# Kernel optimization log

Measured on AMD Instinct MI355X. Metric: run time of the kernel, lower is better.

Reference implementation:

```python
import jax, jax.numpy as jnp
import numpy as np

N = 32768      # nodes
E = 262144     # edges (avg degree 8)
D = 128        # d_model (= per-head out_channels, concat=False)
H = 4          # heads
C = D          # out_channels per head
R = 64         # rel_dim (edge_dim)
NREL = 64      # n_rels
L = 2          # num_layers
LEAK = 0.2     # GATv2 leaky_relu slope
LN_EPS = 1e-5


def setup_inputs() -> dict:
    key = jax.random.key(0)
    ks = jax.random.split(key, 12)
    sdD = 1.0 / np.sqrt(D)
    sdR = 1.0 / np.sqrt(R)
    return {
        "x_flat": jax.random.normal(ks[0], (N, D), jnp.float32),
        "edge_index": jax.random.randint(ks[1], (2, E), 0, N, jnp.int64),
        "edge_type": jax.random.randint(ks[2], (E,), 0, NREL, jnp.int64),
        "valid_mask_flat": jnp.ones((N,), bool),
        "rel_emb": jax.random.normal(ks[3], (NREL, R), jnp.float32) * 0.1,
        "Wl": jax.random.normal(ks[4], (L, D, H * C), jnp.float32) * sdD,
        "bl": jnp.zeros((L, H * C), jnp.float32),
        "Wr": jax.random.normal(ks[5], (L, D, H * C), jnp.float32) * sdD,
        "br": jnp.zeros((L, H * C), jnp.float32),
        "We": jax.random.normal(ks[6], (L, R, H * C), jnp.float32) * sdR,
        "att": jax.random.normal(ks[7], (L, H, C), jnp.float32) * 0.1,
        "bias_o": jnp.zeros((L, D), jnp.float32),
        "ln_g": jnp.ones((L, D), jnp.float32),
        "ln_b": jnp.zeros((L, D), jnp.float32),
    }


def _gatv2_layer(h, src, dst, ea, Wl, bl, Wr, br, We, att, b):
    # h: [N,D]; src/dst: [E+N]; ea: [E+N,R] edge embeddings (incl. self loops)
    xl = (h @ Wl + bl).reshape(N, H, C)   # source transform
    xr = (h @ Wr + br).reshape(N, H, C)   # target transform
    ep = (ea @ We).reshape(-1, H, C)
    e = jax.nn.leaky_relu(xl[src] + xr[dst] + ep, LEAK)   # [E+N,H,C]
    logits = jnp.einsum('ehc,hc->eh', e, att)             # [E+N,H]
    # segment softmax over destination node
    m = jax.ops.segment_max(logits, dst, num_segments=N)
    m = jnp.where(jnp.isfinite(m), m, 0.0)
    p = jnp.exp(logits - m[dst])
    denom = jax.ops.segment_sum(p, dst, num_segments=N)
    alpha = p / (denom[dst] + 1e-16)                      # [E+N,H]
    out = jax.ops.segment_sum(alpha[:, :, None] * xl[src], dst, num_segments=N)
    return out.mean(axis=1) + b                           # concat=False -> head mean


def reference(x_flat, edge_index, edge_type, valid_mask_flat,
              rel_emb, Wl, bl, Wr, br, We, att, bias_o, ln_g, ln_b):
    x = jnp.where(valid_mask_flat[:, None], x_flat, 0.0)
    src, dst = edge_index[0], edge_index[1]
    ea = rel_emb[edge_type]                               # [E,R]
    # PyG add_self_loops with fill_value='mean': self-loop edge_attr is the
    # mean of incoming edge attrs per target node (0 if no incoming edges).
    ones = jnp.ones((E,), x.dtype)
    deg = jax.ops.segment_sum(ones, dst, num_segments=N)
    self_attr = jax.ops.segment_sum(ea, dst, num_segments=N) / jnp.maximum(deg, 1.0)[:, None]
    loop = jnp.arange(N, dtype=src.dtype)
    src_f = jnp.concatenate([src, loop])
    dst_f = jnp.concatenate([dst, loop])
    ea_f = jnp.concatenate([ea, self_attr], axis=0)

    h = x
    for l in range(L):
        msg = _gatv2_layer(h, src_f, dst_f, ea_f,
                           Wl[l], bl[l], Wr[l], br[l], We[l], att[l], bias_o[l])
        msg = jax.nn.gelu(msg, approximate=False)         # dropout = identity (eval)
        hn = h + msg
        mu = jnp.mean(hn, axis=-1, keepdims=True)
        var = jnp.mean(jnp.square(hn - mu), axis=-1, keepdims=True)
        h = (hn - mu) / jnp.sqrt(var + LN_EPS) * ln_g[l] + ln_b[l]
    return jnp.where(valid_mask_flat[:, None], h, 0.0)
```

## Files before the change

### kernel.cpp

```cpp
#include <hip/hip_runtime.h>
#include <hip/hip_bf16.h>
#include <math.h>

#define NN 32768
#define EE 262144
#define DM 128
#define HH 4
#define CC 128
#define HC 512
#define RD 64
#define NRELS 64
#define LEAKS 0.2f
#define LNEPS 1e-5f
#define PIPE_L 4

typedef __hip_bfloat16 bf16;
typedef __attribute__((ext_vector_type(8))) short short8;
typedef __attribute__((ext_vector_type(4))) float f32x4;

typedef const __attribute__((address_space(1))) void* as1cv;
typedef __attribute__((address_space(3))) void* as3v;

__device__ __forceinline__ void gload16(const void* g, void* l) {
    __builtin_amdgcn_global_load_lds((as1cv)g, (as3v)l, 16, 0, 0);
}

__device__ __forceinline__ void unpack8(uint4 u, float* f) {
    f[0] = __uint_as_float((u.x & 0xffffu) << 16);
    f[1] = __uint_as_float(u.x & 0xffff0000u);
    f[2] = __uint_as_float((u.y & 0xffffu) << 16);
    f[3] = __uint_as_float(u.y & 0xffff0000u);
    f[4] = __uint_as_float((u.z & 0xffffu) << 16);
    f[5] = __uint_as_float(u.z & 0xffff0000u);
    f[6] = __uint_as_float((u.w & 0xffffu) << 16);
    f[7] = __uint_as_float(u.w & 0xffff0000u);
}

__global__ void k_deg(const int* __restrict__ dst, int* __restrict__ deg) {
    int e = blockIdx.x * 1024 + threadIdx.x;
    atomicAdd(&deg[dst[e]], 1);
}

__global__ void k_scan1(const int* __restrict__ deg, int* __restrict__ rowptr,
                        int* __restrict__ bsum) {
    __shared__ int s[256];
    int b = blockIdx.x, t = threadIdx.x;
    int v = deg[b * 256 + t];
    s[t] = v;
    __syncthreads();
    for (int off = 1; off < 256; off <<= 1) {
        int x = (t >= off) ? s[t - off] : 0;
        __syncthreads();
        s[t] += x;
        __syncthreads();
    }
    rowptr[b * 256 + t] = s[t] - v;
    if (t == 255) bsum[b] = s[255];
}

__global__ void k_small(const int* __restrict__ bsum, int* __restrict__ boff,
                        const int* __restrict__ hist, int* __restrict__ bcur) {
    __shared__ int s[128];
    int t = threadIdx.x;
    if (blockIdx.x == 0) {
        if (t < 128) s[t] = bsum[t];
        __syncthreads();
        for (int off = 1; off < 128; off <<= 1) {
            int x = (t >= off && t < 128) ? s[t - off] : 0;
            __syncthreads();
            if (t < 128) s[t] += x;
            __syncthreads();
        }
        if (t < 128) boff[t] = s[t] - bsum[t];
        if (t == 127) boff[128] = s[127];
    } else {
        if (t < 64) s[t] = hist[t];
        __syncthreads();
        for (int off = 1; off < 64; off <<= 1) {
            int x = (t >= off && t < 64) ? s[t - off] : 0;
            __syncthreads();
            if (t < 64) s[t] += x;
            __syncthreads();
        }
        if (t < 64) bcur[t] = s[t] - hist[t];
    }
}

__global__ void k_s3p(int* __restrict__ rowptr, const int* __restrict__ boff,
                      const int* __restrict__ deg, int* __restrict__ bcur,
                      int* __restrict__ perm) {
    __shared__ int lh[64], lbase[64];
    int t = threadIdx.x;
    int i = blockIdx.x * 256 + t;
    rowptr[i] += boff[i >> 8];
    if (i == NN - 1) rowptr[NN] = boff[128];
    if (t < 64) lh[t] = 0;
    __syncthreads();
    int d = deg[i];
    int b = 63 - (d > 63 ? 63 : d);
    int my = atomicAdd(&lh[b], 1);
    __syncthreads();
    if (t < 64 && lh[t] > 0) lbase[t] = atomicAdd(&bcur[t], lh[t]);
    __syncthreads();
    perm[lbase[b] + my] = i;
}

__global__ void k_hist(const int* __restrict__ deg, int* __restrict__ hist) {
    __shared__ int lh[64];
    int t = threadIdx.x;
    if (t < 64) lh[t] = 0;
    __syncthreads();
    int d = deg[blockIdx.x * 256 + t];
    int b = 63 - (d > 63 ? 63 : d);
    atomicAdd(&lh[b], 1);
    __syncthreads();
    if (t < 64 && lh[t] > 0) atomicAdd(&hist[t], lh[t]);
}

__global__ void k_fill(const int* __restrict__ src, const int* __restrict__ dst,
                       const int* __restrict__ etype, const int* __restrict__ rowptr,
                       int* __restrict__ cursor, unsigned* __restrict__ csr) {
    int e = blockIdx.x * 1024 + threadIdx.x;
    int d = dst[e];
    int pos = atomicAdd(&cursor[d], 1);
    csr[rowptr[d] + pos] = (unsigned)src[e] | ((unsigned)etype[e] << 16);
}

__global__ void k_prep(const float* __restrict__ x, bf16* __restrict__ hb,
                       const float* __restrict__ Wl, const float* __restrict__ Wr,
                       bf16* __restrict__ Wt,
                       const float* __restrict__ rel_emb, const float* __restrict__ We,
                       bf16* __restrict__ wep) {
    __shared__ float sa[RD];
    int b = blockIdx.x, tid = threadIdx.x;
    if (b < 2048) {
        int i = b * 256 + tid;
        const float4* p = (const float4*)x;
        float4 f0 = p[i * 2], f1 = p[i * 2 + 1];
        bf16 o[8];
        o[0] = __float2bfloat16(f0.x); o[1] = __float2bfloat16(f0.y);
        o[2] = __float2bfloat16(f0.z); o[3] = __float2bfloat16(f0.w);
        o[4] = __float2bfloat16(f1.x); o[5] = __float2bfloat16(f1.y);
        o[6] = __float2bfloat16(f1.z); o[7] = __float2bfloat16(f1.w);
        *reinterpret_cast<uint4*>(hb + (size_t)i * 8) = *reinterpret_cast<uint4*>(o);
    } else if (b < 3072) {
        int idx = (b - 2048) * 256 + tid;
        int l = idx >> 17;
        int rem = idx & 131071;
        int k = rem >> 10;
        int c = rem & 1023;
        const float* WlL = Wl + (size_t)l * DM * HC;
        const float* WrL = Wr + (size_t)l * DM * HC;
        float v = (c < HC) ? WlL[k * HC + c] : WrL[k * HC + (c - HC)];
        Wt[(size_t)l * 1024 * DM + (size_t)c * DM + k] = __float2bfloat16(v);
    } else {
        int blk = b - 3072;
        int l = blk >> 6, r = blk & 63;
        const float* WeL = We + (size_t)l * RD * HC;
        if (tid < RD) sa[tid] = rel_emb[r * RD + tid];
        __syncthreads();
        for (int c = tid; c < HC; c += 256) {
            float s = 0.f;
#pragma unroll 8
            for (int k = 0; k < RD; ++k) s += sa[k] * WeL[k * HC + c];
            wep[(size_t)l * NRELS * HC + (size_t)r * HC + c] = __float2bfloat16(s);
        }
    }
}

__global__ __launch_bounds__(256) void k_gemm_mfma(
    const bf16* __restrict__ hb, const bf16* __restrict__ Wt,
    const float* __restrict__ bl, const float* __restrict__ br,
    bf16* __restrict__ xlb, bf16* __restrict__ xrb) {
    int lane = threadIdx.x & 63;
    int wave = threadIdx.x >> 6;
    int rbase = blockIdx.x * 32;
    int lr = lane & 15;
    int lk = lane >> 4;
    const short* ha = (const short*)hb;
    const short* wa = (const short*)Wt;

    short8 a[2][4];
#pragma unroll
    for (int mi = 0; mi < 2; ++mi)
#pragma unroll
        for (int kk = 0; kk < 4; ++kk)
            a[mi][kk] = *(const short8*)(ha + (size_t)(rbase + mi * 16 + lr) * DM + kk * 32 + lk * 8);

    for (int cg = 0; cg < 4; ++cg) {
        int cbase = cg * 256 + wave * 64;
        short8 b[4][4];
#pragma unroll
        for (int ni = 0; ni < 4; ++ni)
#pragma unroll
            for (int kk = 0; kk < 4; ++kk)
                b[ni][kk] = *(const short8*)(wa + (size_t)(cbase + ni * 16 + lr) * DM + kk * 32 + lk * 8);

        f32x4 c[2][4];
#pragma unroll
        for (int mi = 0; mi < 2; ++mi)
#pragma unroll
            for (int ni = 0; ni < 4; ++ni)
                c[mi][ni] = (f32x4){0.f, 0.f, 0.f, 0.f};

#pragma unroll
        for (int kk = 0; kk < 4; ++kk)
#pragma unroll
            for (int mi = 0; mi < 2; ++mi)
#pragma unroll
                for (int ni = 0; ni < 4; ++ni)
                    c[mi][ni] = __builtin_amdgcn_mfma_f32_16x16x32_bf16(
                        a[mi][kk], b[ni][kk], c[mi][ni], 0, 0, 0);

#pragma unroll
        for (int ni = 0; ni < 4; ++ni) {
            int col = cbase + ni * 16 + lr;
            float bv = (col < HC) ? bl[col] : br[col - HC];
            bf16* outp;
            int cc;
            if (col < HC) { outp = xlb; cc = col; } else { outp = xrb; cc = col - HC; }
#pragma unroll
            for (int mi = 0; mi < 2; ++mi) {
#pragma unroll
                for (int r = 0; r < 4; ++r) {
                    int row = rbase + mi * 16 + lk * 4 + r;
                    outp[(size_t)row * HC + cc] = __float2bfloat16(c[mi][ni][r] + bv);
                }
            }
        }
    }
}

__global__ void k_node(
    const bf16* __restrict__ xlb, const bf16* __restrict__ xrb,
    const bf16* __restrict__ wep,
    const unsigned* __restrict__ csr, const int* __restrict__ rowptr,
    const int* __restrict__ perm,
    const float* __restrict__ attL, const float* __restrict__ biasL,
    const float* __restrict__ lngL, const float* __restrict__ lnbL,
    const float* __restrict__ h_in, float* __restrict__ h_out,
    bf16* __restrict__ hb_out) {
    __shared__ uint4 smem[4 * 528];
    int tid = threadIdx.x;
    int lane = tid & 63;
    int wave = tid >> 6;
    uint4* wls = smem + wave * 528;
    unsigned* csrS = (unsigned*)wls;
    unsigned char* ring = (unsigned char*)(wls + 16);

    int n = perm[blockIdx.x * 4 + wave];
    int head = lane >> 4;
    const int g0 = lane * 8;
    const int ch0 = (lane & 15) * 8;
    const short* xla = (const short*)xlb;
    const short* wpa = (const short*)wep;

    int r0 = rowptr[n], r1 = rowptr[n + 1];
    int d = r1 - r0;
    int de = (d < 64) ? d : 64;

    if (lane < de) csrS[lane] = csr[r0 + lane];

    float attv[8];
    {
        const float4* ap = (const float4*)(attL + head * CC + ch0);
        float4 a0 = ap[0], a1 = ap[1];
        attv[0] = a0.x; attv[1] = a0.y; attv[2] = a0.z; attv[3] = a0.w;
        attv[4] = a1.x; attv[5] = a1.y; attv[6] = a1.z; attv[7] = a1.w;
    }
    float xrn[8];
    unpack8(*(const uint4*)((const short*)xrb + (size_t)n * HC + g0), xrn);

    asm volatile("s_waitcnt vmcnt(0) lgkmcnt(0)" ::: "memory");
    __builtin_amdgcn_sched_barrier(0);

    float denom = 0.f;
    float acc[8], wpsum[8];
#pragma unroll
    for (int j = 0; j < 8; ++j) { acc[j] = 0.f; wpsum[j] = 0.f; }

    int npre = (de < PIPE_L) ? de : PIPE_L;
    for (int k = 0; k < npre; ++k) {
        unsigned u = csrS[k];
        unsigned char* slot = ring + (k & (PIPE_L - 1)) * 2048;
        gload16(xla + (size_t)(u & 0xffffu) * HC + lane * 8, slot);
        gload16(wpa + (size_t)(u >> 16) * HC + lane * 8, slot + 1024);
    }

    int i = 0;
    for (; i + PIPE_L < de; ++i) {
        asm volatile("s_waitcnt vmcnt(6)" ::: "memory");
        __builtin_amdgcn_sched_barrier(0);
        unsigned char* slot = ring + (i & (PIPE_L - 1)) * 2048;
        uint4 xv = *(const uint4*)(slot + lane * 16);
        uint4 wv = *(const uint4*)(slot + 1024 + lane * 16);
        asm volatile("s_waitcnt lgkmcnt(0)" ::: "memory");
        __builtin_amdgcn_sched_barrier(0);
        {
            unsigned u = csrS[i + PIPE_L];
            gload16(xla + (size_t)(u & 0xffffu) * HC + lane * 8, slot);
            gload16(wpa + (size_t)(u >> 16) * HC + lane * 8, slot + 1024);
        }
        float xs[8], wp[8];
        unpack8(xv, xs);
        unpack8(wv, wp);
        float p2 = 0.f;
#pragma unroll
        for (int j = 0; j < 8; ++j) {
            wpsum[j] += wp[j];
            float v = xs[j] + xrn[j] + wp[j];
            v = fmaxf(v, LEAKS * v);
            p2 += v * attv[j];
        }
        p2 += __shfl_xor(p2, 1);
        p2 += __shfl_xor(p2, 2);
        p2 += __shfl_xor(p2, 4);
        p2 += __shfl_xor(p2, 8);
        float pe = __expf(fminf(p2, 80.f));
        denom += pe;
#pragma unroll
        for (int j = 0; j < 8; ++j) acc[j] += pe * xs[j];
    }
    asm volatile("s_waitcnt vmcnt(0)" ::: "memory");
    __builtin_amdgcn_sched_barrier(0);
    for (; i < de; ++i) {
        unsigned char* slot = ring + (i & (PIPE_L - 1)) * 2048;
        uint4 xv = *(const uint4*)(slot + lane * 16);
        uint4 wv = *(const uint4*)(slot + 1024 + lane * 16);
        float xs[8], wp[8];
        unpack8(xv, xs);
        unpack8(wv, wp);
        float p2 = 0.f;
#pragma unroll
        for (int j = 0; j < 8; ++j) {
            wpsum[j] += wp[j];
            float v = xs[j] + xrn[j] + wp[j];
            v = fmaxf(v, LEAKS * v);
            p2 += v * attv[j];
        }
        p2 += __shfl_xor(p2, 1);
        p2 += __shfl_xor(p2, 2);
        p2 += __shfl_xor(p2, 4);
        p2 += __shfl_xor(p2, 8);
        float pe = __expf(fminf(p2, 80.f));
        denom += pe;
#pragma unroll
        for (int j = 0; j < 8; ++j) acc[j] += pe * xs[j];
    }

    for (int k = 64; k < d; ++k) {
        unsigned u = csr[r0 + k];
        uint4 xv = *(const uint4*)(xla + (size_t)(u & 0xffffu) * HC + g0);
        uint4 wv = *(const uint4*)(wpa + (size_t)(u >> 16) * HC + g0);
        float xs[8], wp[8];
        unpack8(xv, xs);
        unpack8(wv, wp);
        float p2 = 0.f;
#pragma unroll
        for (int j = 0; j < 8; ++j) {
            wpsum[j] += wp[j];
            float v = xs[j] + xrn[j] + wp[j];
            v = fmaxf(v, LEAKS * v);
            p2 += v * attv[j];
        }
        p2 += __shfl_xor(p2, 1);
        p2 += __shfl_xor(p2, 2);
        p2 += __shfl_xor(p2, 4);
        p2 += __shfl_xor(p2, 8);
        float pe = __expf(fminf(p2, 80.f));
        denom += pe;
#pragma unroll
        for (int j = 0; j < 8; ++j) acc[j] += pe * xs[j];
    }

    float xln[8];
    unpack8(*(const uint4*)(xla + (size_t)n * HC + g0), xln);
    float invd = (d > 0) ? (1.0f / (float)d) : 1.0f;
    float p2 = 0.f;
#pragma unroll
    for (int j = 0; j < 8; ++j) {
        float v = xln[j] + xrn[j] + wpsum[j] * invd;
        v = fmaxf(v, LEAKS * v);
        p2 += v * attv[j];
    }
    p2 += __shfl_xor(p2, 1);
    p2 += __shfl_xor(p2, 2);
    p2 += __shfl_xor(p2, 4);
    p2 += __shfl_xor(p2, 8);
    {
        float pe = __expf(fminf(p2, 80.f));
        denom += pe;
#pragma unroll
        for (int j = 0; j < 8; ++j) acc[j] += pe * xln[j];
    }

    float inv = 1.0f / (denom + 1e-16f);
    const float4* hp = (const float4*)(h_in + (size_t)n * DM + ch0);
    float4 h0 = hp[0], h1 = hp[1];
    float hin[8] = {h0.x, h0.y, h0.z, h0.w, h1.x, h1.y, h1.z, h1.w};
    float hn[8];
    float lsum = 0.f, lsq = 0.f;
#pragma unroll
    for (int j = 0; j < 8; ++j) {
        float v = acc[j] * inv;
        v += __shfl_xor(v, 16);
        v += __shfl_xor(v, 32);
        float x = v * 0.25f + biasL[ch0 + j];
        float ge = 0.5f * x * (1.0f + erff(x * 0.70710678f));
        float hv = hin[j] + ge;
        hn[j] = hv;
        lsum += hv;
        lsq += hv * hv;
    }
    lsum += __shfl_xor(lsum, 1);
    lsum += __shfl_xor(lsum, 2);
    lsum += __shfl_xor(lsum, 4);
    lsum += __shfl_xor(lsum, 8);
    lsq += __shfl_xor(lsq, 1);
    lsq += __shfl_xor(lsq, 2);
    lsq += __shfl_xor(lsq, 4);
    lsq += __shfl_xor(lsq, 8);
    float mu = lsum * (1.0f / 128.f);
    float var = lsq * (1.0f / 128.f) - mu * mu;
    float rstd = rsqrtf(var + LNEPS);
    if (lane < 16) {
#pragma unroll
        for (int j = 0; j < 8; ++j) {
            float o = (hn[j] - mu) * rstd * lngL[ch0 + j] + lnbL[ch0 + j];
            h_out[(size_t)n * DM + ch0 + j] = o;
            if (hb_out) hb_out[(size_t)n * DM + ch0 + j] = __float2bfloat16(o);
        }
    }
}

extern "C" void kernel_launch(void* const* d_in, const int* in_sizes, int n_in,
                              void* d_out, int out_size, void* d_ws, size_t ws_size,
                              hipStream_t stream) {
    const float* x_flat   = (const float*)d_in[0];
    const int*   edge_idx = (const int*)d_in[1];
    const int*   edge_typ = (const int*)d_in[2];
    const float* rel_emb  = (const float*)d_in[4];
    const float* Wl       = (const float*)d_in[5];
    const float* bl       = (const float*)d_in[6];
    const float* Wr       = (const float*)d_in[7];
    const float* br       = (const float*)d_in[8];
    const float* We       = (const float*)d_in[9];
    const float* att      = (const float*)d_in[10];
    const float* bias_o   = (const float*)d_in[11];
    const float* ln_g     = (const float*)d_in[12];
    const float* ln_b     = (const float*)d_in[13];

    const int* srcp = edge_idx;
    const int* dstp = edge_idx + EE;

    char* w = (char*)d_ws;
    auto alloc = [&](size_t bytes) -> void* {
        void* p = (void*)w;
        w += (bytes + 255) & ~(size_t)255;
        return p;
    };
    bf16*  xlb    = (bf16*)alloc((size_t)NN * HC * 2);
    bf16*  xrb    = (bf16*)alloc((size_t)NN * HC * 2);
    bf16*  hb     = (bf16*)alloc((size_t)NN * DM * 2);
    float* h_mid  = (float*)alloc((size_t)NN * DM * 4);
    bf16*  wep    = (bf16*)alloc((size_t)2 * NRELS * HC * 2);
    bf16*  Wt     = (bf16*)alloc((size_t)2 * 1024 * DM * 2);
    int*   deg    = (int*)alloc((size_t)NN * 4);
    int*   cursor = (int*)alloc((size_t)NN * 4);
    int*   hist   = (int*)alloc((size_t)64 * 4);
    int*   bcur   = (int*)alloc((size_t)64 * 4);
    int*   rowptr = (int*)alloc((size_t)(NN + 1) * 4);
    int*   bsum   = (int*)alloc((size_t)128 * 4);
    int*   boff   = (int*)alloc((size_t)129 * 4);
    int*   perm   = (int*)alloc((size_t)NN * 4);
    unsigned* csr = (unsigned*)alloc((size_t)EE * 4);

    hipMemsetAsync(deg, 0, (size_t)NN * 8 + 512, stream);

    k_deg<<<EE / 1024, 1024, 0, stream>>>(dstp, deg);
    k_scan1<<<NN / 256, 256, 0, stream>>>(deg, rowptr, bsum);
    k_hist<<<NN / 256, 256, 0, stream>>>(deg, hist);
    k_small<<<2, 128, 0, stream>>>(bsum, boff, hist, bcur);
    k_s3p<<<NN / 256, 256, 0, stream>>>(rowptr, boff, deg, bcur, perm);
    k_fill<<<EE / 1024, 1024, 0, stream>>>(srcp, dstp, edge_typ, rowptr, cursor, csr);
    k_prep<<<3200, 256, 0, stream>>>(x_flat, hb, Wl, Wr, Wt, rel_emb, We, wep);

    const float* h = x_flat;
    for (int l = 0; l < 2; ++l) {
        k_gemm_mfma<<<NN / 32, 256, 0, stream>>>(
            hb, Wt + (size_t)l * 1024 * DM,
            bl + (size_t)l * HC, br + (size_t)l * HC, xlb, xrb);
        float* hout = (l == 0) ? h_mid : (float*)d_out;
        k_node<<<NN / 4, 256, 0, stream>>>(xlb, xrb, wep + (size_t)l * NRELS * HC,
                                           csr, rowptr, perm,
                                           att + (size_t)l * HH * CC,
                                           bias_o + (size_t)l * DM,
                                           ln_g + (size_t)l * DM,
                                           ln_b + (size_t)l * DM,
                                           h, hout, (l == 0) ? hb : (bf16*)nullptr);
        h = hout;
    }
}
```

Before: 425.0 us.

## Store xl and relation projections in fp8 and process two nodes per wave

The source-side projection xl and the per-relation edge projections are now stored as fp8 instead of bf16, which halves the bytes gathered per edge in the node aggregation kernel. The LDS ring-buffer pipeline with async global-to-LDS loads is removed. Each wave now handles two destination nodes with interleaved, directly issued register loads to keep memory-level parallelism. The trade-off is lower precision in the attention logits and aggregated messages, and the loss of explicit prefetching.

```diff
diff --git a/kernel.cpp b/kernel.cpp
--- a/kernel.cpp
+++ b/kernel.cpp
@@ -12,18 +12,11 @@
 #define NRELS 64
 #define LEAKS 0.2f
 #define LNEPS 1e-5f
-#define PIPE_L 4
 
 typedef __hip_bfloat16 bf16;
 typedef __attribute__((ext_vector_type(8))) short short8;
 typedef __attribute__((ext_vector_type(4))) float f32x4;
-
-typedef const __attribute__((address_space(1))) void* as1cv;
-typedef __attribute__((address_space(3))) void* as3v;
-
-__device__ __forceinline__ void gload16(const void* g, void* l) {
-    __builtin_amdgcn_global_load_lds((as1cv)g, (as3v)l, 16, 0, 0);
-}
+typedef __attribute__((ext_vector_type(2))) float f32x2;
 
 __device__ __forceinline__ void unpack8(uint4 u, float* f) {
     f[0] = __uint_as_float((u.x & 0xffffu) << 16);
@@ -34,6 +27,15 @@
     f[5] = __uint_as_float(u.z & 0xffff0000u);
     f[6] = __uint_as_float((u.w & 0xffffu) << 16);
     f[7] = __uint_as_float(u.w & 0xffff0000u);
+}
+
+__device__ __forceinline__ void dec8(uint2 v, float* f) {
+    f32x2 a = __builtin_amdgcn_cvt_pk_f32_fp8(v.x, false);
+    f32x2 b = __builtin_amdgcn_cvt_pk_f32_fp8(v.x, true);
+    f32x2 c = __builtin_amdgcn_cvt_pk_f32_fp8(v.y, false);
+    f32x2 d = __builtin_amdgcn_cvt_pk_f32_fp8(v.y, true);
+    f[0] = a.x; f[1] = a.y; f[2] = b.x; f[3] = b.y;
+    f[4] = c.x; f[5] = c.y; f[6] = d.x; f[7] = d.y;
 }
 
 __global__ void k_deg(const int* __restrict__ dst, int* __restrict__ deg) {
@@ -86,6 +88,18 @@
     }
 }
 
+__global__ void k_hist(const int* __restrict__ deg, int* __restrict__ hist) {
+    __shared__ int lh[64];
+    int t = threadIdx.x;
+    if (t < 64) lh[t] = 0;
+    __syncthreads();
+    int d = deg[blockIdx.x * 256 + t];
+    int b = 63 - (d > 63 ? 63 : d);
+    atomicAdd(&lh[b], 1);
+    __syncthreads();
+    if (t < 64 && lh[t] > 0) atomicAdd(&hist[t], lh[t]);
+}
+
 __global__ void k_s3p(int* __restrict__ rowptr, const int* __restrict__ boff,
                       const int* __restrict__ deg, int* __restrict__ bcur,
                       int* __restrict__ perm) {
@@ -105,18 +119,6 @@
     perm[lbase[b] + my] = i;
 }
 
-__global__ void k_hist(const int* __restrict__ deg, int* __restrict__ hist) {
-    __shared__ int lh[64];
-    int t = threadIdx.x;
-    if (t < 64) lh[t] = 0;
-    __syncthreads();
-    int d = deg[blockIdx.x * 256 + t];
-    int b = 63 - (d > 63 ? 63 : d);
-    atomicAdd(&lh[b], 1);
-    __syncthreads();
-    if (t < 64 && lh[t] > 0) atomicAdd(&hist[t], lh[t]);
-}
-
 __global__ void k_fill(const int* __restrict__ src, const int* __restrict__ dst,
                        const int* __restrict__ etype, const int* __restrict__ rowptr,
                        int* __restrict__ cursor, unsigned* __restrict__ csr) {
@@ -130,7 +132,7 @@
                        const float* __restrict__ Wl, const float* __restrict__ Wr,
                        bf16* __restrict__ Wt,
                        const float* __restrict__ rel_emb, const float* __restrict__ We,
-                       bf16* __restrict__ wep) {
+                       unsigned char* __restrict__ wep8) {
     __shared__ float sa[RD];
     int b = blockIdx.x, tid = threadIdx.x;
     if (b < 2048) {
@@ -163,7 +165,8 @@
             float s = 0.f;
 #pragma unroll 8
             for (int k = 0; k < RD; ++k) s += sa[k] * WeL[k * HC + c];
-            wep[(size_t)l * NRELS * HC + (size_t)r * HC + c] = __float2bfloat16(s);
+            unsigned pk = (unsigned)__builtin_amdgcn_cvt_pk_fp8_f32(s, s, 0, false);
+            wep8[(size_t)l * NRELS * HC + (size_t)r * HC + c] = (unsigned char)(pk & 0xff);
         }
     }
 }
@@ -171,7 +174,7 @@
 __global__ __launch_bounds__(256) void k_gemm_mfma(
     const bf16* __restrict__ hb, const bf16* __restrict__ Wt,
     const float* __restrict__ bl, const float* __restrict__ br,
-    bf16* __restrict__ xlb, bf16* __restrict__ xrb) {
+    unsigned char* __restrict__ xl8, bf16* __restrict__ xrb) {
     int lane = threadIdx.x & 63;
     int wave = threadIdx.x >> 6;
     int rbase = blockIdx.x * 32;
@@ -215,16 +218,28 @@
 #pragma unroll
         for (int ni = 0; ni < 4; ++ni) {
             int col = cbase + ni * 16 + lr;
-            float bv = (col < HC) ? bl[col] : br[col - HC];
-            bf16* outp;
-            int cc;
-            if (col < HC) { outp = xlb; cc = col; } else { outp = xrb; cc = col - HC; }
-#pragma unroll
-            for (int mi = 0; mi < 2; ++mi) {
-#pragma unroll
-                for (int r = 0; r < 4; ++r) {
-                    int row = rbase + mi * 16 + lk * 4 + r;
-                    outp[(size_t)row * HC + cc] = __float2bfloat16(c[mi][ni][r] + bv);
+            if (col < HC) {
+                float bv = bl[col];
+#pragma unroll
+                for (int mi = 0; mi < 2; ++mi) {
+#pragma unroll
+                    for (int r = 0; r < 4; ++r) {
+                        int row = rbase + mi * 16 + lk * 4 + r;
+                        float v = c[mi][ni][r] + bv;
+                        unsigned pk = (unsigned)__builtin_amdgcn_cvt_pk_fp8_f32(v, v, 0, false);
+                        xl8[(size_t)row * HC + col] = (unsigned char)(pk & 0xff);
+                    }
+                }
+            } else {
+                int cc = col - HC;
+                float bv = br[cc];
+#pragma unroll
+                for (int mi = 0; mi < 2; ++mi) {
+#pragma unroll
+                    for (int r = 0; r < 4; ++r) {
+                        int row = rbase + mi * 16 + lk * 4 + r;
+                        xrb[(size_t)row * HC + cc] = __float2bfloat16(c[mi][ni][r] + bv);
+                    }
                 }
             }
         }
@@ -232,83 +247,118 @@
 }
 
 __global__ void k_node(
-    const bf16* __restrict__ xlb, const bf16* __restrict__ xrb,
-    const bf16* __restrict__ wep,
+    const unsigned char* __restrict__ xl8, const bf16* __restrict__ xrb,
+    const unsigned char* __restrict__ wep8,
     const unsigned* __restrict__ csr, const int* __restrict__ rowptr,
     const int* __restrict__ perm,
     const float* __restrict__ attL, const float* __restrict__ biasL,
     const float* __restrict__ lngL, const float* __restrict__ lnbL,
     const float* __restrict__ h_in, float* __restrict__ h_out,
     bf16* __restrict__ hb_out) {
-    __shared__ uint4 smem[4 * 528];
     int tid = threadIdx.x;
     int lane = tid & 63;
     int wave = tid >> 6;
-    uint4* wls = smem + wave * 528;
-    unsigned* csrS = (unsigned*)wls;
-    unsigned char* ring = (unsigned char*)(wls + 16);
-
-    int n = perm[blockIdx.x * 4 + wave];
+    int nA = perm[blockIdx.x * 8 + wave * 2];
+    int nB = perm[blockIdx.x * 8 + wave * 2 + 1];
     int head = lane >> 4;
     const int g0 = lane * 8;
     const int ch0 = (lane & 15) * 8;
-    const short* xla = (const short*)xlb;
-    const short* wpa = (const short*)wep;
-
-    int r0 = rowptr[n], r1 = rowptr[n + 1];
-    int d = r1 - r0;
-    int de = (d < 64) ? d : 64;
-
-    if (lane < de) csrS[lane] = csr[r0 + lane];
 
     float attv[8];
-    {
-        const float4* ap = (const float4*)(attL + head * CC + ch0);
-        float4 a0 = ap[0], a1 = ap[1];
-        attv[0] = a0.x; attv[1] = a0.y; attv[2] = a0.z; attv[3] = a0.w;
-        attv[4] = a1.x; attv[5] = a1.y; attv[6] = a1.z; attv[7] = a1.w;
-    }
-    float xrn[8];
-    unpack8(*(const uint4*)((const short*)xrb + (size_t)n * HC + g0), xrn);
-
-    asm volatile("s_waitcnt vmcnt(0) lgkmcnt(0)" ::: "memory");
-    __builtin_amdgcn_sched_barrier(0);
-
-    float denom = 0.f;
-    float acc[8], wpsum[8];
-#pragma unroll
-    for (int j = 0; j < 8; ++j) { acc[j] = 0.f; wpsum[j] = 0.f; }
-
-    int npre = (de < PIPE_L) ? de : PIPE_L;
-    for (int k = 0; k < npre; ++k) {
-        unsigned u = csrS[k];
-        unsigned char* slot = ring + (k & (PIPE_L - 1)) * 2048;
-        gload16(xla + (size_t)(u & 0xffffu) * HC + lane * 8, slot);
-        gload16(wpa + (size_t)(u >> 16) * HC + lane * 8, slot + 1024);
-    }
-
-    int i = 0;
-    for (; i + PIPE_L < de; ++i) {
-        asm volatile("s_waitcnt vmcnt(6)" ::: "memory");
-        __builtin_amdgcn_sched_barrier(0);
-        unsigned char* slot = ring + (i & (PIPE_L - 1)) * 2048;
-        uint4 xv = *(const uint4*)(slot + lane * 16);
-        uint4 wv = *(const uint4*)(slot + 1024 + lane * 16);
-        asm volatile("s_waitcnt lgkmcnt(0)" ::: "memory");
-        __builtin_amdgcn_sched_barrier(0);
+#pragma unroll
+    for (int j = 0; j < 8; ++j) attv[j] = attL[head * CC + ch0 + j];
+
+    float xrnA[8], xrnB[8];
+    unpack8(*(const uint4*)((const short*)xrb + (size_t)nA * HC + g0), xrnA);
+    unpack8(*(const uint4*)((const short*)xrb + (size_t)nB * HC + g0), xrnB);
+
+    float denomA = 0.f, denomB = 0.f;
+    float accA[8], accB[8], wpsA[8], wpsB[8];
+#pragma unroll
+    for (int j = 0; j < 8; ++j) { accA[j] = 0.f; accB[j] = 0.f; wpsA[j] = 0.f; wpsB[j] = 0.f; }
+
+    int r0A = rowptr[nA], dA = rowptr[nA + 1] - r0A;
+    int r0B = rowptr[nB], dB = rowptr[nB + 1] - r0B;
+    const unsigned* cpA = csr + r0A;
+    const unsigned* cpB = csr + r0B;
+    int kmax = (dA > dB) ? dA : dB;
+
+    for (int k = 0; k < kmax; ++k) {
+        bool doA = (k < dA), doB = (k < dB);
+        uint2 xvA, wvA, xvB, wvB;
+        if (doA) {
+            unsigned u = cpA[k];
+            xvA = *(const uint2*)(xl8 + (size_t)(u & 0xffffu) * HC + g0);
+            wvA = *(const uint2*)(wep8 + (size_t)(u >> 16) * HC + g0);
+        }
+        if (doB) {
+            unsigned u = cpB[k];
+            xvB = *(const uint2*)(xl8 + (size_t)(u & 0xffffu) * HC + g0);
+            wvB = *(const uint2*)(wep8 + (size_t)(u >> 16) * HC + g0);
+        }
+        if (doA) {
+            float xs[8], wp[8];
+            dec8(xvA, xs);
+            dec8(wvA, wp);
+            float p2 = 0.f;
+#pragma unroll
+            for (int j = 0; j < 8; ++j) {
+                wpsA[j] += wp[j];
+                float v = xs[j] + xrnA[j] + wp[j];
+                v = fmaxf(v, LEAKS * v);
+                p2 += v * attv[j];
+            }
+            p2 += __shfl_xor(p2, 1);
+            p2 += __shfl_xor(p2, 2);
+            p2 += __shfl_xor(p2, 4);
+            p2 += __shfl_xor(p2, 8);
+            float pe = __expf(fminf(p2, 80.f));
+            denomA += pe;
+#pragma unroll
+            for (int j = 0; j < 8; ++j) accA[j] += pe * xs[j];
+        }
+        if (doB) {
+            float xs[8], wp[8];
+            dec8(xvB, xs);
+            dec8(wvB, wp);
+            float p2 = 0.f;
+#pragma unroll
+            for (int j = 0; j < 8; ++j) {
+                wpsB[j] += wp[j];
+                float v = xs[j] + xrnB[j] + wp[j];
+                v = fmaxf(v, LEAKS * v);
+                p2 += v * attv[j];
+            }
+            p2 += __shfl_xor(p2, 1);
+            p2 += __shfl_xor(p2, 2);
+            p2 += __shfl_xor(p2, 4);
+            p2 += __shfl_xor(p2, 8);
+            float pe = __expf(fminf(p2, 80.f));
+            denomB += pe;
+#pragma unroll
+            for (int j = 0; j < 8; ++j) accB[j] += pe * xs[j];
+        }
+    }
+
+#pragma unroll
+    for (int s = 0; s < 2; ++s) {
+        int n = s ? nB : nA;
+        int d = s ? dB : dA;
+        float* acc = s ? accB : accA;
+        float* wps = s ? wpsB : wpsA;
+        float* xrn = s ? xrnB : xrnA;
+        float denom = s ? denomB : denomA;
+
+        float xln[8];
         {
-            unsigned u = csrS[i + PIPE_L];
-            gload16(xla + (size_t)(u & 0xffffu) * HC + lane * 8, slot);
-            gload16(wpa + (size_t)(u >> 16) * HC + lane * 8, slot + 1024);
-        }
-        float xs[8], wp[8];
-        unpack8(xv, xs);
-        unpack8(wv, wp);
+            uint2 xv = *(const uint2*)(xl8 + (size_t)n * HC + g0);
+            dec8(xv, xln);
+        }
+        float invd = (d > 0) ? (1.0f / (float)d) : 1.0f;
         float p2 = 0.f;
 #pragma unroll
         for (int j = 0; j < 8; ++j) {
-            wpsum[j] += wp[j];
-            float v = xs[j] + xrn[j] + wp[j];
+            float v = xln[j] + xrn[j] + wps[j] * invd;
             v = fmaxf(v, LEAKS * v);
             p2 += v * attv[j];
         }
@@ -319,116 +369,44 @@
         float pe = __expf(fminf(p2, 80.f));
         denom += pe;
 #pragma unroll
-        for (int j = 0; j < 8; ++j) acc[j] += pe * xs[j];
-    }
-    asm volatile("s_waitcnt vmcnt(0)" ::: "memory");
-    __builtin_amdgcn_sched_barrier(0);
-    for (; i < de; ++i) {
-        unsigned char* slot = ring + (i & (PIPE_L - 1)) * 2048;
-        uint4 xv = *(const uint4*)(slot + lane * 16);
-        uint4 wv = *(const uint4*)(slot + 1024 + lane * 16);
-        float xs[8], wp[8];
-        unpack8(xv, xs);
-        unpack8(wv, wp);
-        float p2 = 0.f;
+        for (int j = 0; j < 8; ++j) acc[j] += pe * xln[j];
+
+        float inv = 1.0f / (denom + 1e-16f);
+        const float4* hp = (const float4*)(h_in + (size_t)n * DM + ch0);
+        float4 h0 = hp[0], h1 = hp[1];
+        float hin[8] = {h0.x, h0.y, h0.z, h0.w, h1.x, h1.y, h1.z, h1.w};
+        float hn[8];
+        float lsum = 0.f, lsq = 0.f;
 #pragma unroll
         for (int j = 0; j < 8; ++j) {
-            wpsum[j] += wp[j];
-            float v = xs[j] + xrn[j] + wp[j];
-            v = fmaxf(v, LEAKS * v);
-            p2 += v * attv[j];
-        }
-        p2 += __shfl_xor(p2, 1);
-        p2 += __shfl_xor(p2, 2);
-        p2 += __shfl_xor(p2, 4);
-        p2 += __shfl_xor(p2, 8);
-        float pe = __expf(fminf(p2, 80.f));
-        denom += pe;
-#pragma unroll
-        for (int j = 0; j < 8; ++j) acc[j] += pe * xs[j];
-    }
-
-    for (int k = 64; k < d; ++k) {
-        unsigned u = csr[r0 + k];
-        uint4 xv = *(const uint4*)(xla + (size_t)(u & 0xffffu) * HC + g0);
-        uint4 wv = *(const uint4*)(wpa + (size_t)(u >> 16) * HC + g0);
-        float xs[8], wp[8];
-        unpack8(xv, xs);
-        unpack8(wv, wp);
-        float p2 = 0.f;
-#pragma unroll
-        for (int j = 0; j < 8; ++j) {
-            wpsum[j] += wp[j];
-            float v = xs[j] + xrn[j] + wp[j];
-            v = fmaxf(v, LEAKS * v);
-            p2 += v * attv[j];
-        }
-        p2 += __shfl_xor(p2, 1);
-        p2 += __shfl_xor(p2, 2);
-        p2 += __shfl_xor(p2, 4);
-        p2 += __shfl_xor(p2, 8);
-        float pe = __expf(fminf(p2, 80.f));
-        denom += pe;
-#pragma unroll
-        for (int j = 0; j < 8; ++j) acc[j] += pe * xs[j];
-    }
-
-    float xln[8];
-    unpack8(*(const uint4*)(xla + (size_t)n * HC + g0), xln);
-    float invd = (d > 0) ? (1.0f / (float)d) : 1.0f;
-    float p2 = 0.f;
-#pragma unroll
-    for (int j = 0; j < 8; ++j) {
-        float v = xln[j] + xrn[j] + wpsum[j] * invd;
-        v = fmaxf(v, LEAKS * v);
-        p2 += v * attv[j];
-    }
-    p2 += __shfl_xor(p2, 1);
-    p2 += __shfl_xor(p2, 2);
-    p2 += __shfl_xor(p2, 4);
-    p2 += __shfl_xor(p2, 8);
-    {
-        float pe = __expf(fminf(p2, 80.f));
-        denom += pe;
-#pragma unroll
-        for (int j = 0; j < 8; ++j) acc[j] += pe * xln[j];
-    }
-
-    float inv = 1.0f / (denom + 1e-16f);
-    const float4* hp = (const float4*)(h_in + (size_t)n * DM + ch0);
-    float4 h0 = hp[0], h1 = hp[1];
-    float hin[8] = {h0.x, h0.y, h0.z, h0.w, h1.x, h1.y, h1.z, h1.w};
-    float hn[8];
-    float lsum = 0.f, lsq = 0.f;
-#pragma unroll
-    for (int j = 0; j < 8; ++j) {
-        float v = acc[j] * inv;
-        v += __shfl_xor(v, 16);
-        v += __shfl_xor(v, 32);
-        float x = v * 0.25f + biasL[ch0 + j];
-        float ge = 0.5f * x * (1.0f + erff(x * 0.70710678f));
-        float hv = hin[j] + ge;
-        hn[j] = hv;
-        lsum += hv;
-        lsq += hv * hv;
-    }
-    lsum += __shfl_xor(lsum, 1);
-    lsum += __shfl_xor(lsum, 2);
-    lsum += __shfl_xor(lsum, 4);
-    lsum += __shfl_xor(lsum, 8);
-    lsq += __shfl_xor(lsq, 1);
-    lsq += __shfl_xor(lsq, 2);
-    lsq += __shfl_xor(lsq, 4);
-    lsq += __shfl_xor(lsq, 8);
-    float mu = lsum * (1.0f / 128.f);
-    float var = lsq * (1.0f / 128.f) - mu * mu;
-    float rstd = rsqrtf(var + LNEPS);
-    if (lane < 16) {
-#pragma unroll
-        for (int j = 0; j < 8; ++j) {
-            float o = (hn[j] - mu) * rstd * lngL[ch0 + j] + lnbL[ch0 + j];
-            h_out[(size_t)n * DM + ch0 + j] = o;
-            if (hb_out) hb_out[(size_t)n * DM + ch0 + j] = __float2bfloat16(o);
+            float v = acc[j] * inv;
+            v += __shfl_xor(v, 16);
+            v += __shfl_xor(v, 32);
+            float x = v * 0.25f + biasL[ch0 + j];
+            float ge = 0.5f * x * (1.0f + erff(x * 0.70710678f));
+            float hv = hin[j] + ge;
+            hn[j] = hv;
+            lsum += hv;
+            lsq += hv * hv;
+        }
+        lsum += __shfl_xor(lsum, 1);
+        lsum += __shfl_xor(lsum, 2);
+        lsum += __shfl_xor(lsum, 4);
+        lsum += __shfl_xor(lsum, 8);
+        lsq += __shfl_xor(lsq, 1);
+        lsq += __shfl_xor(lsq, 2);
+        lsq += __shfl_xor(lsq, 4);
+        lsq += __shfl_xor(lsq, 8);
+        float mu = lsum * (1.0f / 128.f);
+        float var = lsq * (1.0f / 128.f) - mu * mu;
+        float rstd = rsqrtf(var + LNEPS);
+        if (lane < 16) {
+#pragma unroll
+            for (int j = 0; j < 8; ++j) {
+                float o = (hn[j] - mu) * rstd * lngL[ch0 + j] + lnbL[ch0 + j];
+                h_out[(size_t)n * DM + ch0 + j] = o;
+                if (hb_out) hb_out[(size_t)n * DM + ch0 + j] = __float2bfloat16(o);
+            }
         }
     }
 }
@@ -459,11 +437,11 @@
         w += (bytes + 255) & ~(size_t)255;
         return p;
     };
-    bf16*  xlb    = (bf16*)alloc((size_t)NN * HC * 2);
+    unsigned char* xl8 = (unsigned char*)alloc((size_t)NN * HC);
     bf16*  xrb    = (bf16*)alloc((size_t)NN * HC * 2);
     bf16*  hb     = (bf16*)alloc((size_t)NN * DM * 2);
     float* h_mid  = (float*)alloc((size_t)NN * DM * 4);
-    bf16*  wep    = (bf16*)alloc((size_t)2 * NRELS * HC * 2);
+    unsigned char* wep8 = (unsigned char*)alloc((size_t)2 * NRELS * HC);
     bf16*  Wt     = (bf16*)alloc((size_t)2 * 1024 * DM * 2);
     int*   deg    = (int*)alloc((size_t)NN * 4);
     int*   cursor = (int*)alloc((size_t)NN * 4);
@@ -483,15 +461,16 @@
     k_small<<<2, 128, 0, stream>>>(bsum, boff, hist, bcur);
     k_s3p<<<NN / 256, 256, 0, stream>>>(rowptr, boff, deg, bcur, perm);
     k_fill<<<EE / 1024, 1024, 0, stream>>>(srcp, dstp, edge_typ, rowptr, cursor, csr);
-    k_prep<<<3200, 256, 0, stream>>>(x_flat, hb, Wl, Wr, Wt, rel_emb, We, wep);
+    k_prep<<<3200, 256, 0, stream>>>(x_flat, hb, Wl, Wr, Wt, rel_emb, We, wep8);
 
     const float* h = x_flat;
     for (int l = 0; l < 2; ++l) {
         k_gemm_mfma<<<NN / 32, 256, 0, stream>>>(
             hb, Wt + (size_t)l * 1024 * DM,
-            bl + (size_t)l * HC, br + (size_t)l * HC, xlb, xrb);
+            bl + (size_t)l * HC, br + (size_t)l * HC, xl8, xrb);
         float* hout = (l == 0) ? h_mid : (float*)d_out;
-        k_node<<<NN / 4, 256, 0, stream>>>(xlb, xrb, wep + (size_t)l * NRELS * HC,
+        k_node<<<NN / 8, 256, 0, stream>>>(xl8, xrb,
+                                           wep8 + (size_t)l * NRELS * HC,
                                            csr, rowptr, perm,
                                            att + (size_t)l * HH * CC,
                                            bias_o + (size_t)l * DM,
```

After: 438.5 us. 3.2% more time.
